# Kernel optimization log

Hardware: AMD Instinct MI355X
Metric: run time of the kernel (lower is better)

Reference implementation:

```python
import jax, jax.numpy as jnp
import numpy as np

N, D, K = 32768, 64, 8192

def setup_inputs() -> dict:
    key = jax.random.key(0)
    k1, k2 = jax.random.split(key)
    x = jax.random.normal(k1, (N, D), dtype=jnp.float32)
    w = jax.random.normal(k2, (D, K), dtype=jnp.float32)  # codebook: (embedding_dim, num_embeddings)
    return {"x": x, "w": w}

def reference(x, w):
    distances = (
        jnp.sum(x * x, axis=1, keepdims=True)
        - 2.0 * (x @ w)
        + jnp.sum(w * w, axis=0, keepdims=True)
    )  # [N, K]
    encoding_indices = jnp.argmin(distances, axis=1)  # [N] (argmax of -distances)
    # quantize: embedding_lookup on w^T  -> [N, D]
    quantized = jnp.take(w.T, encoding_indices, axis=0)
    return quantized
```

## Files before the change

kernel.cpp:

```cpp
#include <hip/hip_runtime.h>
#include <hip/hip_bf16.h>
#include <hip/hip_fp16.h>
#include <cstdint>
#include <cstddef>

#define NROWS 32768
#define DDIM  64
#define KDIM  8192
#define DELTA 1.25f

typedef float  f32x4 __attribute__((ext_vector_type(4)));
typedef short  s16x8 __attribute__((ext_vector_type(8)));
typedef unsigned long long u64;


__device__ __forceinline__ uint32_t fmono(float f) {
    uint32_t u = __float_as_uint(f);
    return (u & 0x80000000u) ? ~u : (u | 0x80000000u);
}


__global__ void __launch_bounds__(256)
vq_prep_w(const float* __restrict__ w, ushort* __restrict__ wtb,
          float* __restrict__ wt, float4* __restrict__ wt4,
          float* __restrict__ wsq) {
    __shared__ float tile[64][65];
    const int kbase = blockIdx.x * 64;
    const int t = threadIdx.x, wv = t >> 6, lane = t & 63;
    const int l15 = lane & 15, l4 = (lane >> 4) & 3;
#pragma unroll
    for (int it = 0; it < 16; ++it) {
        int d = it * 4 + wv;
        tile[lane][d] = w[(size_t)d * KDIM + kbase + lane];
    }
    __syncthreads();
#pragma unroll
    for (int h = 0; h < 2; ++h) {
        s16x8 c;
#pragma unroll
        for (int e = 0; e < 8; ++e) {
            float v = -2.0f * tile[wv * 16 + l15][h * 32 + l4 * 8 + e];
            __hip_bfloat16 hb = __float2bfloat16(v);
            c[e] = *(short*)&hb;
        }
        ((s16x8*)wtb)[(size_t)(blockIdx.x * 4 + wv) * 128 + h * 64 + lane] = c;
    }
#pragma unroll
    for (int it = 0; it < 16; ++it) {
        int kk = it * 4 + wv;
        wt[(size_t)(kbase + kk) * DDIM + lane] = tile[kk][lane];
    }
#pragma unroll
    for (int it = 0; it < 4; ++it) {
        int i = wv * 4 + it;
        float4 v;
        v.x = tile[lane][i * 4 + 0];
        v.y = tile[lane][i * 4 + 1];
        v.z = tile[lane][i * 4 + 2];
        v.w = tile[lane][i * 4 + 3];
        wt4[(size_t)i * KDIM + kbase + lane] = v;
    }
    if (wv == 0) {
        float s = 0.f;
#pragma unroll
        for (int d = 0; d < DDIM; ++d) {
            float v = tile[lane][d];
            s = fmaf(v, v, s);
        }
        wsq[kbase + lane] = s;
    }
}

__global__ void __launch_bounds__(256)
vq_prep_x(const float* __restrict__ x, ushort* __restrict__ xb) {
    const int t = threadIdx.x, wv = t >> 6, lane = t & 63;
    const int l15 = lane & 15, l4 = (lane >> 4) & 3;
    const int r = blockIdx.x * 64 + wv * 16 + l15;
#pragma unroll
    for (int h = 0; h < 2; ++h) {
        const float* src = &x[(size_t)r * DDIM + h * 32 + l4 * 8];
        float4 a = *(const float4*)src;
        float4 b = *(const float4*)(src + 4);
        float fv[8] = {a.x, a.y, a.z, a.w, b.x, b.y, b.z, b.w};
        s16x8 c;
#pragma unroll
        for (int e = 0; e < 8; ++e) {
            __hip_bfloat16 hb = __float2bfloat16(fv[e]);
            c[e] = *(short*)&hb;
        }
        ((s16x8*)xb)[(size_t)(blockIdx.x * 4 + wv) * 128 + h * 64 + lane] = c;
    }
}

__global__ void __launch_bounds__(256)
vq_scoreA(const ushort* __restrict__ xb, const ushort* __restrict__ wb,
          const float* __restrict__ wsq, ushort* __restrict__ lsub) {
    const int t = threadIdx.x, wv = t >> 6, lane = t & 63;
    const int l15 = lane & 15, l4 = lane >> 4;
    const int rbase = (blockIdx.x >> 3) * 128;
    const int kg    = (blockIdx.x & 7) * 4 + wv;
    const int kbase = kg * 256;

    const s16x8* xs  = (const s16x8*)xb;
    const s16x8* wsx = (const s16x8*)wb;

    s16x8 bfrag[8][2];
#pragma unroll
    for (int rt = 0; rt < 8; ++rt)
#pragma unroll
        for (int h = 0; h < 2; ++h)
            bfrag[rt][h] = xs[(size_t)((rbase >> 4) + rt) * 128 + h * 64 + lane];

#pragma unroll
    for (int sub = 0; sub < 4; ++sub) {
        const int kw = kbase + sub * 64;

        s16x8 afrag[4][2];
#pragma unroll
        for (int kt = 0; kt < 4; ++kt)
#pragma unroll
            for (int h = 0; h < 2; ++h)
                afrag[kt][h] = wsx[(size_t)((kw >> 4) + kt) * 128 + h * 64 + lane];

        f32x4 wq[4];
#pragma unroll
        for (int kt = 0; kt < 4; ++kt)
            wq[kt] = *(const f32x4*)&wsq[kw + kt * 16 + l4 * 4];

#pragma unroll
        for (int rt = 0; rt < 8; ++rt) {
            f32x4 acc[4];
#pragma unroll
            for (int kt = 0; kt < 4; ++kt) acc[kt] = wq[kt];
#pragma unroll
            for (int kt = 0; kt < 4; ++kt) {
                acc[kt] = __builtin_amdgcn_mfma_f32_16x16x32_bf16(afrag[kt][0], bfrag[rt][0], acc[kt], 0, 0, 0);
                acc[kt] = __builtin_amdgcn_mfma_f32_16x16x32_bf16(afrag[kt][1], bfrag[rt][1], acc[kt], 0, 0, 0);
            }
            float g0 = fminf(fminf(acc[0][0], acc[0][1]), acc[0][2]);
            float g1 = fminf(fminf(acc[0][3], acc[1][0]), acc[1][1]);
            float g2 = fminf(fminf(acc[1][2], acc[1][3]), acc[2][0]);
            float g3 = fminf(fminf(acc[2][1], acc[2][2]), acc[2][3]);
            float g4 = fminf(fminf(acc[3][0], acc[3][1]), acc[3][2]);
            float h0 = fminf(fminf(g0, g1), g2);
            float h1 = fminf(fminf(g3, g4), acc[3][3]);
            float m  = fminf(h0, h1);
            m = fminf(m, __shfl_xor(m, 16));
            m = fminf(m, __shfl_xor(m, 32));
            if (l4 == 0) {
                __half hh = __float2half(m);
                lsub[(size_t)(rbase + rt * 16 + l15) * 128 + kg * 4 + sub] =
                    *(ushort*)&hh;
            }
        }
    }
}

__global__ void __launch_bounds__(64)
vq_finish(const float* __restrict__ x, const float4* __restrict__ wt4,
          const float* __restrict__ wt, const float* __restrict__ wsq,
          const ushort* __restrict__ lsub, float* __restrict__ out) {
    const int lane = threadIdx.x;
    const int row  = blockIdx.x;

    ushort2 us = ((const ushort2*)(lsub + (size_t)row * 128))[lane];
    float v0 = __half2float(*(__half*)&us.x);
    float v1 = __half2float(*(__half*)&us.y);
    float m = fminf(v0, v1);
#pragma unroll
    for (int o = 1; o < 64; o <<= 1) m = fminf(m, __shfl_xor(m, o));
    const float thr = m + DELTA;
    u64 b0 = __ballot(v0 <= thr);
    u64 b1 = __ballot(v1 <= thr);

    float xs[64];
    const float4* xp = (const float4*)(x + (size_t)row * DDIM);
#pragma unroll
    for (int i = 0; i < 16; ++i) {
        float4 v = xp[i];
        xs[4 * i + 0] = v.x;
        xs[4 * i + 1] = v.y;
        xs[4 * i + 2] = v.z;
        xs[4 * i + 3] = v.w;
    }

    u64 best = ~0ull;
#pragma unroll
    for (int half = 0; half < 2; ++half) {
        u64 b = half ? b1 : b0;
        while (b) {
            int s = __ffsll(b) - 1;
            b &= b - 1;
            const int kk = (s * 2 + half) * 64 + lane;
            float qq = wsq[kk];
            const float4* wr = wt4 + kk;
            float a0 = 0.f, a1 = 0.f, a2 = 0.f, a3 = 0.f;
#pragma unroll
            for (int i = 0; i < 16; ++i) {
                float4 wv4 = wr[(size_t)i * KDIM];
                a0 = fmaf(xs[4 * i + 0], wv4.x, a0);
                a1 = fmaf(xs[4 * i + 1], wv4.y, a1);
                a2 = fmaf(xs[4 * i + 2], wv4.z, a2);
                a3 = fmaf(xs[4 * i + 3], wv4.w, a3);
            }
            float dot = (a0 + a1) + (a2 + a3);
            float sc  = fmaf(-2.f, dot, qq);
            u64 key = ((u64)fmono(sc) << 32) | (unsigned)kk;
            best = (key < best) ? key : best;
        }
    }
#pragma unroll
    for (int sh = 1; sh < 64; sh <<= 1) {
        u64 o = __shfl_xor(best, sh);
        best = (o < best) ? o : best;
    }
    const int bk = (int)(best & 0xFFFFFFFFull);
    out[(size_t)row * DDIM + lane] = wt[(size_t)bk * DDIM + lane];
}


#define BR 128
#define BK 128
#define DPH 32
typedef float v2f __attribute__((ext_vector_type(2)));

__global__ void fb_prep(const float* __restrict__ w, float* __restrict__ wt,
                        float* __restrict__ wsq) {
    int k = blockIdx.x * blockDim.x + threadIdx.x;
    if (k >= KDIM) return;
    float s = 0.f;
#pragma unroll
    for (int d = 0; d < DDIM; ++d) {
        float v = w[(size_t)d * KDIM + k];
        wt[(size_t)k * DDIM + d] = v;
        s = fmaf(v, v, s);
    }
    wsq[k] = s;
}
__global__ void fb_init(u64* __restrict__ keys) {
    int i = blockIdx.x * blockDim.x + threadIdx.x;
    if (i < NROWS) keys[i] = ~0ull;
}
__global__ void __launch_bounds__(256, 4)
fb_gemm(const float* __restrict__ x, const float* __restrict__ w,
        const float* __restrict__ wsq, u64* __restrict__ keys) {
    __shared__ float xT[DPH][BR];
    __shared__ float wl[DPH][BK];
    const int kblk  = blockIdx.x & (KDIM / BK - 1);
    const int rbase = (blockIdx.x >> 6) * BR;
    const int kbase = kblk * BK;
    const int t     = threadIdx.x;
    const int wave = t >> 6, lane = t & 63;
    const int rg = lane >> 3, cg = lane & 7;
    const int xoff = (wave >> 1) * 64 + rg * 8;
    const int coff = (wave & 1) * 64 + cg * 8;
    v2f acc[8][4];
#pragma unroll
    for (int i = 0; i < 8; ++i)
#pragma unroll
        for (int j = 0; j < 4; ++j) acc[i][j] = (v2f)(0.f);
#pragma unroll
    for (int p = 0; p < 2; ++p) {
        {
            const int row = t & 127, dgrp = t >> 7;
#pragma unroll
            for (int it = 0; it < 4; ++it) {
                const int dl = (dgrp + it * 2) * 4;
                float4 v = *(const float4*)&x[(size_t)(rbase + row) * DDIM + p * DPH + dl];
                xT[dl + 0][row] = v.x; xT[dl + 1][row] = v.y;
                xT[dl + 2][row] = v.z; xT[dl + 3][row] = v.w;
            }
        }
        {
#pragma unroll
            for (int it = 0; it < 4; ++it) {
                const int o4 = t + it * 256;
                const int dl = o4 >> 5, c4 = (o4 & 31) << 2;
                float4 v = *(const float4*)&w[(size_t)(p * DPH + dl) * KDIM + kbase + c4];
                *(float4*)&wl[dl][c4] = v;
            }
        }
        __syncthreads();
#pragma unroll 4
        for (int d = 0; d < DPH; ++d) {
            float4 xa = *(const float4*)&xT[d][xoff];
            float4 xb = *(const float4*)&xT[d][xoff + 4];
            float4 wa = *(const float4*)&wl[d][coff];
            float4 wb = *(const float4*)&wl[d][coff + 4];
            v2f wv0 = {wa.x, wa.y}, wv1 = {wa.z, wa.w};
            v2f wv2 = {wb.x, wb.y}, wv3 = {wb.z, wb.w};
            float xrr[8] = {xa.x, xa.y, xa.z, xa.w, xb.x, xb.y, xb.z, xb.w};
#pragma unroll
            for (int i = 0; i < 8; ++i) {
                v2f xsV = {xrr[i], xrr[i]};
                acc[i][0] = __builtin_elementwise_fma(xsV, wv0, acc[i][0]);
                acc[i][1] = __builtin_elementwise_fma(xsV, wv1, acc[i][1]);
                acc[i][2] = __builtin_elementwise_fma(xsV, wv2, acc[i][2]);
                acc[i][3] = __builtin_elementwise_fma(xsV, wv3, acc[i][3]);
            }
        }
        __syncthreads();
    }
    const int kc = kbase + coff;
    float4 qa = *(const float4*)&wsq[kc];
    float4 qb = *(const float4*)&wsq[kc + 4];
    v2f q2[4] = {{qa.x, qa.y}, {qa.z, qa.w}, {qb.x, qb.y}, {qb.z, qb.w}};
    const v2f neg2 = {-2.f, -2.f};
#pragma unroll
    for (int i = 0; i < 8; ++i) {
        float sc[8];
#pragma unroll
        for (int jj = 0; jj < 4; ++jj) {
            v2f s2 = __builtin_elementwise_fma(neg2, acc[i][jj], q2[jj]);
            sc[2 * jj] = s2.x; sc[2 * jj + 1] = s2.y;
        }
        float bestv = sc[0]; int bj = 0;
#pragma unroll
        for (int j = 1; j < 8; ++j)
            if (sc[j] < bestv) { bestv = sc[j]; bj = j; }
        u64 key = ((u64)fmono(bestv) << 32) | (unsigned)(kc + bj);
        u64 o;
        o = __shfl_xor(key, 1); key = (o < key) ? o : key;
        o = __shfl_xor(key, 2); key = (o < key) ? o : key;
        o = __shfl_xor(key, 4); key = (o < key) ? o : key;
        if (cg == 0) atomicMin(&keys[rbase + xoff + i], key);
    }
}
__global__ void fb_gather(const u64* __restrict__ keys,
                          const float* __restrict__ wt,
                          float* __restrict__ out) {
    int t = blockIdx.x * blockDim.x + threadIdx.x;
    if (t >= NROWS * DDIM) return;
    int row = t >> 6;
    int d   = t & 63;
    int k   = (int)(keys[row] & 0xFFFFFFFFull);
    out[t] = wt[(size_t)k * DDIM + d];
}


extern "C" void kernel_launch(void* const* d_in, const int* in_sizes, int n_in,
                              void* d_out, int out_size, void* d_ws, size_t ws_size,
                              hipStream_t stream) {
    const float* x = (const float*)d_in[0];
    const float* w = (const float*)d_in[1];
    float* out = (float*)d_out;

    char* ws = (char*)d_ws;
    const size_t OFF_WTB  = 0;
    const size_t OFF_WSQ  = 1048576;
    const size_t OFF_XB   = 1081344;
    const size_t OFF_WT   = 5275648;
    const size_t OFF_WT4  = 7372800;
    const size_t OFF_LSUB = 9469952;
    const size_t NEED     = 17858560;

    if (ws_size >= NEED) {
        ushort* wtb  = (ushort*)(ws + OFF_WTB);
        float*  wsq  = (float*)(ws + OFF_WSQ);
        ushort* xbb  = (ushort*)(ws + OFF_XB);
        float*  wt   = (float*)(ws + OFF_WT);
        float4* wt4  = (float4*)(ws + OFF_WT4);
        ushort* lsub = (ushort*)(ws + OFF_LSUB);

        vq_prep_w<<<KDIM / 64, 256, 0, stream>>>(w, wtb, wt, wt4, wsq);
        vq_prep_x<<<NROWS / 64, 256, 0, stream>>>(x, xbb);
        vq_scoreA<<<(NROWS / 128) * 8, 256, 0, stream>>>(xbb, wtb, wsq, lsub);
        vq_finish<<<NROWS, 64, 0, stream>>>(x, wt4, wt, wsq, lsub, out);
    } else {
        float* wt  = (float*)ws;
        float* wsq = (float*)(ws + 2097152);
        u64*   keys = (u64*)(ws + 2129920);
        fb_prep<<<KDIM / 256, 256, 0, stream>>>(w, wt, wsq);
        fb_init<<<NROWS / 256, 256, 0, stream>>>(keys);
        fb_gemm<<<(NROWS / BR) * (KDIM / BK), 256, 0, stream>>>(x, w, wsq, keys);
        fb_gather<<<(NROWS * DDIM) / 256, 256, 0, stream>>>(keys, wt, out);
    }
}
```

Before: 86.85 us.

## Merge prep kernels, reorder score grid, and pack partial-min stores

Combines the codebook and input preparation kernels into one launch that dispatches on block index, removing one kernel launch and its serialization gap. The score kernel's block mapping is swapped so consecutive blocks share the same codebook group and walk different row tiles. The per-row half-precision minima for the four sub-chunks are accumulated in registers and written as a single 64-bit store instead of four scattered 16-bit stores. The cost is extra register pressure for the packed values and a different cache access pattern for codebook and input fragments.

```diff
diff --git a/kernel.cpp b/kernel.cpp
--- a/kernel.cpp
+++ b/kernel.cpp
@@ -21,74 +21,75 @@
 
 
 __global__ void __launch_bounds__(256)
-vq_prep_w(const float* __restrict__ w, ushort* __restrict__ wtb,
-          float* __restrict__ wt, float4* __restrict__ wt4,
-          float* __restrict__ wsq) {
+vq_prep(const float* __restrict__ w, const float* __restrict__ x,
+        ushort* __restrict__ wtb, float* __restrict__ wt,
+        float4* __restrict__ wt4, float* __restrict__ wsq,
+        ushort* __restrict__ xb) {
     __shared__ float tile[64][65];
-    const int kbase = blockIdx.x * 64;
     const int t = threadIdx.x, wv = t >> 6, lane = t & 63;
     const int l15 = lane & 15, l4 = (lane >> 4) & 3;
-#pragma unroll
-    for (int it = 0; it < 16; ++it) {
-        int d = it * 4 + wv;
-        tile[lane][d] = w[(size_t)d * KDIM + kbase + lane];
-    }
-    __syncthreads();
-#pragma unroll
-    for (int h = 0; h < 2; ++h) {
-        s16x8 c;
-#pragma unroll
-        for (int e = 0; e < 8; ++e) {
-            float v = -2.0f * tile[wv * 16 + l15][h * 32 + l4 * 8 + e];
-            __hip_bfloat16 hb = __float2bfloat16(v);
-            c[e] = *(short*)&hb;
-        }
-        ((s16x8*)wtb)[(size_t)(blockIdx.x * 4 + wv) * 128 + h * 64 + lane] = c;
-    }
-#pragma unroll
-    for (int it = 0; it < 16; ++it) {
-        int kk = it * 4 + wv;
-        wt[(size_t)(kbase + kk) * DDIM + lane] = tile[kk][lane];
-    }
-#pragma unroll
-    for (int it = 0; it < 4; ++it) {
-        int i = wv * 4 + it;
-        float4 v;
-        v.x = tile[lane][i * 4 + 0];
-        v.y = tile[lane][i * 4 + 1];
-        v.z = tile[lane][i * 4 + 2];
-        v.w = tile[lane][i * 4 + 3];
-        wt4[(size_t)i * KDIM + kbase + lane] = v;
-    }
-    if (wv == 0) {
-        float s = 0.f;
-#pragma unroll
-        for (int d = 0; d < DDIM; ++d) {
-            float v = tile[lane][d];
-            s = fmaf(v, v, s);
-        }
-        wsq[kbase + lane] = s;
-    }
-}
-
-__global__ void __launch_bounds__(256)
-vq_prep_x(const float* __restrict__ x, ushort* __restrict__ xb) {
-    const int t = threadIdx.x, wv = t >> 6, lane = t & 63;
-    const int l15 = lane & 15, l4 = (lane >> 4) & 3;
-    const int r = blockIdx.x * 64 + wv * 16 + l15;
-#pragma unroll
-    for (int h = 0; h < 2; ++h) {
-        const float* src = &x[(size_t)r * DDIM + h * 32 + l4 * 8];
-        float4 a = *(const float4*)src;
-        float4 b = *(const float4*)(src + 4);
-        float fv[8] = {a.x, a.y, a.z, a.w, b.x, b.y, b.z, b.w};
-        s16x8 c;
-#pragma unroll
-        for (int e = 0; e < 8; ++e) {
-            __hip_bfloat16 hb = __float2bfloat16(fv[e]);
-            c[e] = *(short*)&hb;
-        }
-        ((s16x8*)xb)[(size_t)(blockIdx.x * 4 + wv) * 128 + h * 64 + lane] = c;
+
+    if (blockIdx.x < KDIM / 64) {
+        const int bid = blockIdx.x;
+        const int kbase = bid * 64;
+#pragma unroll
+        for (int it = 0; it < 16; ++it) {
+            int d = it * 4 + wv;
+            tile[lane][d] = w[(size_t)d * KDIM + kbase + lane];
+        }
+        __syncthreads();
+#pragma unroll
+        for (int h = 0; h < 2; ++h) {
+            s16x8 c;
+#pragma unroll
+            for (int e = 0; e < 8; ++e) {
+                float v = -2.0f * tile[wv * 16 + l15][h * 32 + l4 * 8 + e];
+                __hip_bfloat16 hb = __float2bfloat16(v);
+                c[e] = *(short*)&hb;
+            }
+            ((s16x8*)wtb)[(size_t)(bid * 4 + wv) * 128 + h * 64 + lane] = c;
+        }
+#pragma unroll
+        for (int it = 0; it < 16; ++it) {
+            int kk = it * 4 + wv;
+            wt[(size_t)(kbase + kk) * DDIM + lane] = tile[kk][lane];
+        }
+#pragma unroll
+        for (int it = 0; it < 4; ++it) {
+            int i = wv * 4 + it;
+            float4 v;
+            v.x = tile[lane][i * 4 + 0];
+            v.y = tile[lane][i * 4 + 1];
+            v.z = tile[lane][i * 4 + 2];
+            v.w = tile[lane][i * 4 + 3];
+            wt4[(size_t)i * KDIM + kbase + lane] = v;
+        }
+        if (wv == 0) {
+            float s = 0.f;
+#pragma unroll
+            for (int d = 0; d < DDIM; ++d) {
+                float v = tile[lane][d];
+                s = fmaf(v, v, s);
+            }
+            wsq[kbase + lane] = s;
+        }
+    } else {
+        const int bid = blockIdx.x - KDIM / 64;
+        const int r = bid * 64 + wv * 16 + l15;
+#pragma unroll
+        for (int h = 0; h < 2; ++h) {
+            const float* src = &x[(size_t)r * DDIM + h * 32 + l4 * 8];
+            float4 a = *(const float4*)src;
+            float4 b = *(const float4*)(src + 4);
+            float fv[8] = {a.x, a.y, a.z, a.w, b.x, b.y, b.z, b.w};
+            s16x8 c;
+#pragma unroll
+            for (int e = 0; e < 8; ++e) {
+                __hip_bfloat16 hb = __float2bfloat16(fv[e]);
+                c[e] = *(short*)&hb;
+            }
+            ((s16x8*)xb)[(size_t)(bid * 4 + wv) * 128 + h * 64 + lane] = c;
+        }
     }
 }
 
@@ -97,8 +98,8 @@
           const float* __restrict__ wsq, ushort* __restrict__ lsub) {
     const int t = threadIdx.x, wv = t >> 6, lane = t & 63;
     const int l15 = lane & 15, l4 = lane >> 4;
-    const int rbase = (blockIdx.x >> 3) * 128;
-    const int kg    = (blockIdx.x & 7) * 4 + wv;
+    const int rbase = (blockIdx.x & 255) * 128;
+    const int kg    = (blockIdx.x >> 8) * 4 + wv;
     const int kbase = kg * 256;
 
     const s16x8* xs  = (const s16x8*)xb;
@@ -110,6 +111,10 @@
 #pragma unroll
         for (int h = 0; h < 2; ++h)
             bfrag[rt][h] = xs[(size_t)((rbase >> 4) + rt) * 128 + h * 64 + lane];
+
+    u64 packs[8];
+#pragma unroll
+    for (int rt = 0; rt < 8; ++rt) packs[rt] = 0ull;
 
 #pragma unroll
     for (int sub = 0; sub < 4; ++sub) {
@@ -147,12 +152,15 @@
             float m  = fminf(h0, h1);
             m = fminf(m, __shfl_xor(m, 16));
             m = fminf(m, __shfl_xor(m, 32));
-            if (l4 == 0) {
-                __half hh = __float2half(m);
-                lsub[(size_t)(rbase + rt * 16 + l15) * 128 + kg * 4 + sub] =
-                    *(ushort*)&hh;
-            }
-        }
+            __half hh = __float2half(m);
+            packs[rt] |= (u64)(*(ushort*)&hh) << (16 * sub);
+        }
+    }
+
+    if (l4 == 0) {
+#pragma unroll
+        for (int rt = 0; rt < 8; ++rt)
+            *(u64*)&lsub[(size_t)(rbase + rt * 16 + l15) * 128 + kg * 4] = packs[rt];
     }
 }
 
@@ -362,8 +370,7 @@
         float4* wt4  = (float4*)(ws + OFF_WT4);
         ushort* lsub = (ushort*)(ws + OFF_LSUB);
 
-        vq_prep_w<<<KDIM / 64, 256, 0, stream>>>(w, wtb, wt, wt4, wsq);
-        vq_prep_x<<<NROWS / 64, 256, 0, stream>>>(x, xbb);
+        vq_prep<<<KDIM / 64 + NROWS / 64, 256, 0, stream>>>(w, x, wtb, wt, wt4, wsq, xbb);
         vq_scoreA<<<(NROWS / 128) * 8, 256, 0, stream>>>(xbb, wtb, wsq, lsub);
         vq_finish<<<NROWS, 64, 0, stream>>>(x, wt4, wt, wsq, lsub, out);
     } else {
```

After: 80.48 us, median of 2. 1.08x faster.
